# Kernel optimization log

Hardware: AMD Instinct MI355X
Metric: run time of the kernel (lower is better)

Reference implementation:

```python
import jax, jax.numpy as jnp
import numpy as np

KERNEL_SIZE = 4  # kernel_size=4, dim=1, degree-1 open B-splines (SplineConv defaults)


def spline_conv(x, edge_index, edge_attr, W, root, bias):
    """SplineConv with dim=1, kernel_size=4, degree=1, open splines, aggr='mean'.

    x: [N, F_in]; edge_index: [2, E] (row 0 = source, row 1 = target);
    edge_attr: [E, 1] pseudo-coords in [0,1]; W: [K, F_in, F_out];
    root: [F_in, F_out]; bias: [F_out].
    """
    N = x.shape[0]
    src, dst = edge_index[0], edge_index[1]
    u = edge_attr[:, 0]                          # [E]
    v = u * (KERNEL_SIZE - 1)                    # open spline: scale by K-1
    vf = jnp.floor(v)
    frac = v - vf                                # [E], degree-1 basis fraction
    k0 = jnp.clip(vf.astype(jnp.int32), 0, KERNEL_SIZE - 1)
    k1 = jnp.minimum(k0 + 1, KERNEL_SIZE - 1)
    # Project node features through all K kernel weights once: [N, K, F_out]
    xw = jnp.einsum('nf,kfo->nko', x, W)
    # Per-edge message: basis-weighted mix of the two active kernel projections
    m = (1.0 - frac)[:, None] * xw[src, k0] + frac[:, None] * xw[src, k1]  # [E, F_out]
    # Mean aggregation at target nodes
    agg = jax.ops.segment_sum(m, dst, num_segments=N)               # [N, F_out]
    deg = jax.ops.segment_sum(jnp.ones_like(u), dst, num_segments=N)
    agg = agg / jnp.maximum(deg, 1.0)[:, None]
    return agg + x @ root + bias


def setup_inputs() -> dict:
    key = jax.random.key(0)
    ks = jax.random.split(key, 9)
    N, E, F_IN, HID, C = 50000, 1600000, 48, 32, 10
    x = jax.random.normal(ks[0], (N, F_IN), dtype=jnp.float32)
    edge_index = jax.random.randint(ks[1], (2, E), 0, N, dtype=jnp.int64)
    edge_attr = jax.random.uniform(ks[2], (E, 1), dtype=jnp.float32)
    s = 0.1
    W1 = jax.random.normal(ks[3], (KERNEL_SIZE, F_IN, HID), dtype=jnp.float32) * s
    root1 = jax.random.normal(ks[4], (F_IN, HID), dtype=jnp.float32) * s
    bias1 = jax.random.normal(ks[5], (HID,), dtype=jnp.float32) * s
    W2 = jax.random.normal(ks[6], (KERNEL_SIZE, HID, C), dtype=jnp.float32) * s
    root2 = jax.random.normal(ks[7], (HID, C), dtype=jnp.float32) * s
    bias2 = jax.random.normal(ks[8], (C,), dtype=jnp.float32) * s
    return {"x": x, "edge_index": edge_index, "edge_attr": edge_attr,
            "W1": W1, "root1": root1, "bias1": bias1,
            "W2": W2, "root2": root2, "bias2": bias2}


def reference(x, edge_index, edge_attr, W1, root1, bias1, W2, root2, bias2):
    # dropout is identity in eval mode (training=self.training)
    h = spline_conv(x, edge_index, edge_attr, W1, root1, bias1)
    h = jax.nn.elu(h)
    h = spline_conv(h, edge_index, edge_attr, W2, root2, bias2)
    return jax.nn.log_softmax(h, axis=1)
```

## Files before the change

### kernel.cpp

```cpp
#include <hip/hip_runtime.h>
#include <math.h>


#define F_IN   48
#define HID    32
#define NCLS   10
#define KS     4
#define BKT_SH 8
#define TILE   4096

__device__ inline unsigned short f2bf(float f) {
    unsigned x = __float_as_uint(f);
    unsigned r = x + 0x7FFFu + ((x >> 16) & 1u);
    return (unsigned short)(r >> 16);
}
__device__ inline float bf2f(unsigned short u) {
    return __uint_as_float(((unsigned)u) << 16);
}


__global__ void bucket_hist_kernel(const int* __restrict__ ei, int* __restrict__ bcnt,
                                   int E, int NB) {
    __shared__ int lcnt[256];
    int t = threadIdx.x;
    lcnt[t] = 0;
    __syncthreads();
    int e0 = blockIdx.x * TILE;
    int n = min(TILE, E - e0);
    for (int r = 0; r < TILE / 256; ++r) {
        int i = r * 256 + t;
        if (i < n) atomicAdd(&lcnt[ei[E + e0 + i] >> BKT_SH], 1);
    }
    __syncthreads();
    if (t < NB && lcnt[t] > 0) atomicAdd(&bcnt[t], lcnt[t]);
}

__global__ void mini_scan_kernel(const int* __restrict__ bcnt, int* __restrict__ bbase,
                                 int* __restrict__ gcur, int NB) {
    __shared__ int a[256], c[256];
    int t = threadIdx.x;
    int v = (t < NB) ? bcnt[t] : 0;
    a[t] = v; c[t] = v;
    __syncthreads();
    for (int o = 1; o < 256; o <<= 1) {
        int w = (t >= o) ? a[t - o] : 0;
        __syncthreads();
        a[t] += w;
        __syncthreads();
    }
    int ex = a[t] - c[t];
    if (t < NB) { bbase[t] = ex; gcur[t] = ex; }
    if (t == 0) bbase[NB] = a[255];
}

__global__ void bucket_scatter_kernel(const int* __restrict__ ei, const float* __restrict__ ea,
                                      int* __restrict__ gcur, uint2* __restrict__ tpd,
                                      int E, int NB) {
    __shared__ unsigned spl[TILE];
    __shared__ unsigned short sdst[TILE];
    __shared__ unsigned short inv[TILE];
    __shared__ int lcnt[256], loff[256], lrank[256], gb[256];
    int t = threadIdx.x;
    lcnt[t] = 0; lrank[t] = 0;
    __syncthreads();
    int e0 = blockIdx.x * TILE;
    int n = min(TILE, E - e0);
    for (int r = 0; r < TILE / 256; ++r) {
        int i = r * 256 + t;
        if (i < n) {
            int e = e0 + i;
            int src = ei[e];
            int dst = ei[E + e];
            float u = ea[e];
            float v = u * (float)(KS - 1);
            float vf = floorf(v);
            int k0 = min(max((int)vf, 0), KS - 1);
            unsigned qf = (unsigned)((v - vf) * 16383.f + 0.5f);
            spl[i] = (unsigned)src | ((unsigned)k0 << 16) | (qf << 18);
            sdst[i] = (unsigned short)dst;
            atomicAdd(&lcnt[dst >> BKT_SH], 1);
        }
    }
    __syncthreads();
    loff[t] = lcnt[t];
    __syncthreads();
    for (int o = 1; o < 256; o <<= 1) {
        int w = (t >= o) ? loff[t - o] : 0;
        __syncthreads();
        loff[t] += w;
        __syncthreads();
    }
    int ex = loff[t] - lcnt[t];
    __syncthreads();
    loff[t] = ex;
    if (t < NB) gb[t] = atomicAdd(&gcur[t], lcnt[t]);
    __syncthreads();
    for (int r = 0; r < TILE / 256; ++r) {
        int i = r * 256 + t;
        if (i < n) {
            int b = sdst[i] >> BKT_SH;
            int p = loff[b] + atomicAdd(&lrank[b], 1);
            inv[p] = (unsigned short)i;
        }
    }
    __syncthreads();
    for (int r = 0; r < TILE / 256; ++r) {
        int j = r * 256 + t;
        if (j < n) {
            int i = inv[j];
            int d = sdst[i];
            int b = d >> BKT_SH;
            int pos = gb[b] + (j - loff[b]);
            tpd[pos] = make_uint2(spl[i], (unsigned)d);
        }
    }
}

__global__ void node_sort_kernel(const uint2* __restrict__ tpd, const int* __restrict__ bbase,
                                 unsigned* __restrict__ spk, int* __restrict__ offs,
                                 int N, int NB) {
    __shared__ int hc[256], hs[256], hr[256];
    int b = blockIdx.x;
    int t = threadIdx.x;
    int nb0 = b << BKT_SH;
    int nb = min(256, N - nb0);
    int base = bbase[b];
    int m = bbase[b + 1] - base;
    hc[t] = 0; hr[t] = 0;
    __syncthreads();
    for (int i = t; i < m; i += 256) atomicAdd(&hc[tpd[base + i].y - nb0], 1);
    __syncthreads();
    hs[t] = hc[t];
    __syncthreads();
    for (int o = 1; o < 256; o <<= 1) {
        int w = (t >= o) ? hs[t - o] : 0;
        __syncthreads();
        hs[t] += w;
        __syncthreads();
    }
    if (t < nb) offs[nb0 + t] = base + (hs[t] - hc[t]);
    if (b == NB - 1 && t == 0) offs[N] = base + m;
    for (int i = t; i < m; i += 256) {
        uint2 rec = tpd[base + i];
        int d = rec.y - nb0;
        int p = (hs[d] - hc[d]) + atomicAdd(&hr[d], 1);
        spk[base + p] = rec.x;
    }
}


__global__ __launch_bounds__(320) void xw1_kernel(
        const float* __restrict__ X, const float* __restrict__ W,
        const float* __restrict__ R, unsigned short* __restrict__ outk,
        float* __restrict__ outr, int n) {
    __shared__ float lw[48 * 160];
    int t = threadIdx.x;
    for (int i = t; i < 48 * 160; i += 320) {
        int f = i / 160;
        int col = i - f * 160;
        lw[i] = (col < 128) ? W[(size_t)(col >> 5) * (48 * 32) + f * 32 + (col & 31)]
                            : R[f * 32 + (col - 128)];
    }
    __syncthreads();
    int g = t % 40;
    int lp = t / 40;
    int n0 = (blockIdx.x * 8 + lp) * 2;
    if (n0 + 1 >= n) return;
    const float4* X0 = (const float4*)(X + (size_t)n0 * F_IN);
    const float4* X1 = (const float4*)(X + (size_t)(n0 + 1) * F_IN);
    float4 x0[12], x1[12];
#pragma unroll
    for (int i = 0; i < 12; ++i) { x0[i] = X0[i]; x1[i] = X1[i]; }
    const float4* lw4 = (const float4*)lw;
    float4 a0 = {0,0,0,0}, a1 = {0,0,0,0};
#pragma unroll
    for (int fb = 0; fb < 12; ++fb) {
        float4 v0 = x0[fb], v1 = x1[fb];
#pragma unroll
        for (int j = 0; j < 4; ++j) {
            float s0 = (j == 0) ? v0.x : (j == 1) ? v0.y : (j == 2) ? v0.z : v0.w;
            float s1 = (j == 0) ? v1.x : (j == 1) ? v1.y : (j == 2) ? v1.z : v1.w;
            float4 w = lw4[(fb * 4 + j) * 40 + g];
            a0.x = fmaf(s0, w.x, a0.x); a0.y = fmaf(s0, w.y, a0.y);
            a0.z = fmaf(s0, w.z, a0.z); a0.w = fmaf(s0, w.w, a0.w);
            a1.x = fmaf(s1, w.x, a1.x); a1.y = fmaf(s1, w.y, a1.y);
            a1.z = fmaf(s1, w.z, a1.z); a1.w = fmaf(s1, w.w, a1.w);
        }
    }
    if (g < 32) {
        uint2 u0, u1;
        u0.x = f2bf(a0.x) | ((unsigned)f2bf(a0.y) << 16);
        u0.y = f2bf(a0.z) | ((unsigned)f2bf(a0.w) << 16);
        u1.x = f2bf(a1.x) | ((unsigned)f2bf(a1.y) << 16);
        u1.y = f2bf(a1.z) | ((unsigned)f2bf(a1.w) << 16);
        *(uint2*)(outk + (size_t)n0 * (KS * HID) + g * 4) = u0;
        *(uint2*)(outk + (size_t)(n0 + 1) * (KS * HID) + g * 4) = u1;
    } else {
        int o = 4 * g - 128;
        *(float4*)(outr + (size_t)n0 * HID + o) = a0;
        *(float4*)(outr + (size_t)(n0 + 1) * HID + o) = a1;
    }
}

__global__ void xw2_kernel(const float* __restrict__ H, const float* __restrict__ W,
                           const float* __restrict__ R, unsigned short* __restrict__ outk,
                           float* __restrict__ outr, int n) {
    __shared__ float lw2[32 * 50];
    int t = threadIdx.x;
    for (int i = t; i < 32 * 50; i += 256) {
        int f = i / 50;
        int col = i - f * 50;
        lw2[i] = (col < 40) ? W[(size_t)(col / 10) * (32 * 10) + f * 10 + (col % 10)]
                            : R[f * 10 + (col - 40)];
    }
    __syncthreads();
    int total = (n / 2) * 25;
    int id = blockIdx.x * blockDim.x + t;
    if (id >= total) return;
    int p = id % 25;
    int pr = id / 25;
    int n0 = 2 * pr;
    const float4* H0 = (const float4*)(H + (size_t)n0 * HID);
    const float4* H1 = (const float4*)(H + (size_t)(n0 + 1) * HID);
    float4 h0[8], h1[8];
#pragma unroll
    for (int i = 0; i < 8; ++i) { h0[i] = H0[i]; h1[i] = H1[i]; }
    const float2* lwp = (const float2*)lw2;
    float ax0 = 0.f, ay0 = 0.f, ax1 = 0.f, ay1 = 0.f;
#pragma unroll
    for (int fb = 0; fb < 8; ++fb) {
        float4 v0 = h0[fb], v1 = h1[fb];
#pragma unroll
        for (int j = 0; j < 4; ++j) {
            float s0 = (j == 0) ? v0.x : (j == 1) ? v0.y : (j == 2) ? v0.z : v0.w;
            float s1 = (j == 0) ? v1.x : (j == 1) ? v1.y : (j == 2) ? v1.z : v1.w;
            float2 w = lwp[(fb * 4 + j) * 25 + p];
            ax0 = fmaf(s0, w.x, ax0); ay0 = fmaf(s0, w.y, ay0);
            ax1 = fmaf(s1, w.x, ax1); ay1 = fmaf(s1, w.y, ay1);
        }
    }
    int col = 2 * p;
    if (col < KS * NCLS) {
        *(unsigned*)(outk + (size_t)n0 * (KS * NCLS) + col) =
            f2bf(ax0) | ((unsigned)f2bf(ay0) << 16);
        *(unsigned*)(outk + (size_t)(n0 + 1) * (KS * NCLS) + col) =
            f2bf(ax1) | ((unsigned)f2bf(ay1) << 16);
    } else {
        int o = col - KS * NCLS;
        *(float2*)(outr + (size_t)n0 * NCLS + o) = make_float2(ax0, ay0);
        *(float2*)(outr + (size_t)(n0 + 1) * NCLS + o) = make_float2(ax1, ay1);
    }
}


__device__ inline float interp32(const unsigned short* __restrict__ xwk, unsigned p, int c) {
    int src = p & 0xFFFF;
    int k0 = (p >> 16) & 3;
    int k1 = min(k0 + 1, KS - 1);
    float fr = (float)(p >> 18) * (1.f / 16383.f);
    const unsigned short* row = xwk + (size_t)src * (KS * HID);
    float v0 = bf2f(row[k0 * HID + c]);
    float v1 = bf2f(row[k1 * HID + c]);
    return fmaf(fr, v1 - v0, v0);
}

__global__ void agg1_kernel(const unsigned short* __restrict__ xwk,
                            const float* __restrict__ xroot,
                            const int* __restrict__ offs, const unsigned* __restrict__ spk,
                            const float* __restrict__ bias, float* __restrict__ h, int n) {
    int lane = threadIdx.x & 63;
    int c = lane & 31;
    int half = lane >> 5;
    int node = blockIdx.x * 4 + (threadIdx.x >> 6);
    if (node >= n) return;
    int beg = offs[node];
    int end = offs[node + 1];
    float s0 = 0.f, s1 = 0.f;
    int e = beg + half;
    while (e + 2 < end) {
        unsigned p0 = spk[e];
        unsigned p1 = spk[e + 2];
        s0 += interp32(xwk, p0, c);
        s1 += interp32(xwk, p1, c);
        e += 4;
    }
    if (e < end) s0 += interp32(xwk, spk[e], c);
    float sum = s0 + s1;
    sum += __shfl_xor(sum, 32, 64);
    int deg = end - beg;
    float m = sum / (float)(deg > 0 ? deg : 1);
    float o = m + xroot[(size_t)node * HID + c] + bias[c];
    if (half == 0) h[(size_t)node * HID + c] = (o > 0.f) ? o : expm1f(o);
}

__device__ inline float interp10(const unsigned short* __restrict__ xwk, unsigned p, int cc) {
    int src = p & 0xFFFF;
    int k0 = (p >> 16) & 3;
    int k1 = min(k0 + 1, KS - 1);
    float fr = (float)(p >> 18) * (1.f / 16383.f);
    const unsigned short* row = xwk + (size_t)src * (KS * NCLS);
    float v0 = bf2f(row[k0 * NCLS + cc]);
    float v1 = bf2f(row[k1 * NCLS + cc]);
    return fmaf(fr, v1 - v0, v0);
}

__global__ void agg2_kernel(const unsigned short* __restrict__ xwk,
                            const float* __restrict__ xroot,
                            const int* __restrict__ offs, const unsigned* __restrict__ spk,
                            const float* __restrict__ bias, float* __restrict__ out, int n) {
    int g = threadIdx.x & 31;
    int c = g & 15;
    int par = g >> 4;
    int node = blockIdx.x * 8 + (threadIdx.x >> 5);
    if (node >= n) return;
    int cc = min(c, NCLS - 1);
    int beg = offs[node];
    int end = offs[node + 1];
    float s0 = 0.f, s1 = 0.f;
    int e = beg + par;
    while (e + 2 < end) {
        unsigned p0 = spk[e];
        unsigned p1 = spk[e + 2];
        s0 += interp10(xwk, p0, cc);
        s1 += interp10(xwk, p1, cc);
        e += 4;
    }
    if (e < end) s0 += interp10(xwk, spk[e], cc);
    float sum = s0 + s1;
    sum += __shfl_xor(sum, 16, 32);
    int deg = end - beg;
    float m = sum / (float)(deg > 0 ? deg : 1);
    float logit = m + xroot[(size_t)node * NCLS + cc] + bias[cc];
    bool active = (c < NCLS);
    float mx = active ? logit : -INFINITY;
#pragma unroll
    for (int msk = 1; msk < 16; msk <<= 1) mx = fmaxf(mx, __shfl_xor(mx, msk, 16));
    float ex = active ? expf(logit - mx) : 0.f;
    float s = ex;
#pragma unroll
    for (int msk = 1; msk < 16; msk <<= 1) s += __shfl_xor(s, msk, 16);
    if (active && par == 0) out[(size_t)node * NCLS + c] = (logit - mx) - logf(s);
}

extern "C" void kernel_launch(void* const* d_in, const int* in_sizes, int n_in,
                              void* d_out, int out_size, void* d_ws, size_t ws_size,
                              hipStream_t stream) {
    const float* x       = (const float*)d_in[0];
    const int*   ei      = (const int*)d_in[1];
    const float* ea      = (const float*)d_in[2];
    const float* W1      = (const float*)d_in[3];
    const float* root1   = (const float*)d_in[4];
    const float* bias1   = (const float*)d_in[5];
    const float* W2      = (const float*)d_in[6];
    const float* root2   = (const float*)d_in[7];
    const float* bias2   = (const float*)d_in[8];
    float* out = (float*)d_out;

    const int N = in_sizes[0] / F_IN;
    const int E = in_sizes[2];
    const int NB = (N + 255) >> BKT_SH;

    char* base = (char*)d_ws;
    size_t off = 0;
    auto alloc = [&](size_t bytes) {
        char* p = base + off;
        off = (off + bytes + 255) & ~(size_t)255;
        return (void*)p;
    };
    unsigned short* xwk1 = (unsigned short*)alloc((size_t)N * KS * HID * 2);
    float* xr1           = (float*)alloc((size_t)N * HID * 4);
    float* h             = (float*)alloc((size_t)N * HID * 4);
    int* offs            = (int*)alloc(((size_t)N + 1) * 4);
    int* bcnt            = (int*)alloc((size_t)NB * 4);
    int* bbase           = (int*)alloc(((size_t)NB + 1) * 4);
    int* gcur            = (int*)alloc((size_t)NB * 4);
    unsigned* spk        = (unsigned*)alloc((size_t)E * 4);
    uint2* tpd           = (uint2*)xwk1;
    unsigned short* xwk2 = xwk1;
    float* xr2           = xr1;
    if (ws_size < off) return;

    int ebk = (E + TILE - 1) / TILE;

    hipMemsetAsync(bcnt, 0, (size_t)NB * 4, stream);
    bucket_hist_kernel<<<ebk, 256, 0, stream>>>(ei, bcnt, E, NB);
    mini_scan_kernel<<<1, 256, 0, stream>>>(bcnt, bbase, gcur, NB);
    bucket_scatter_kernel<<<ebk, 256, 0, stream>>>(ei, ea, gcur, tpd, E, NB);
    node_sort_kernel<<<NB, 256, 0, stream>>>(tpd, bbase, spk, offs, N, NB);
    xw1_kernel<<<(N + 15) / 16, 320, 0, stream>>>(x, W1, root1, xwk1, xr1, N);
    agg1_kernel<<<(N + 3) / 4, 256, 0, stream>>>(xwk1, xr1, offs, spk, bias1, h, N);
    {
        int total = (N / 2) * 25;
        xw2_kernel<<<(total + 255) / 256, 256, 0, stream>>>(h, W2, root2, xwk2, xr2, N);
    }
    agg2_kernel<<<(N + 7) / 8, 256, 0, stream>>>(xwk2, xr2, offs, spk, bias2, out, N);
}
```

Before: 266.7 us.

## Drop per-node sort; aggregate bucketed edges with shared-memory atomics per block

Removes the node_sort pass that built a CSR layout. Both aggregation kernels now run one 1024-thread block per 256-node bucket, read the bucketed edge records directly, and accumulate messages into shared-memory tiles with atomic adds. Degrees are counted in the first pass and reused in the second. This saves a sort pass and the CSR indirection, but adds heavy LDS atomic contention and gives only 196 blocks, so the GPU may be underfilled. The edge buffer now needs its own workspace allocation instead of aliasing xwk1.

```diff
diff --git a/kernel.cpp b/kernel.cpp
--- a/kernel.cpp
+++ b/kernel.cpp
@@ -116,38 +116,6 @@
     }
 }
 
-__global__ void node_sort_kernel(const uint2* __restrict__ tpd, const int* __restrict__ bbase,
-                                 unsigned* __restrict__ spk, int* __restrict__ offs,
-                                 int N, int NB) {
-    __shared__ int hc[256], hs[256], hr[256];
-    int b = blockIdx.x;
-    int t = threadIdx.x;
-    int nb0 = b << BKT_SH;
-    int nb = min(256, N - nb0);
-    int base = bbase[b];
-    int m = bbase[b + 1] - base;
-    hc[t] = 0; hr[t] = 0;
-    __syncthreads();
-    for (int i = t; i < m; i += 256) atomicAdd(&hc[tpd[base + i].y - nb0], 1);
-    __syncthreads();
-    hs[t] = hc[t];
-    __syncthreads();
-    for (int o = 1; o < 256; o <<= 1) {
-        int w = (t >= o) ? hs[t - o] : 0;
-        __syncthreads();
-        hs[t] += w;
-        __syncthreads();
-    }
-    if (t < nb) offs[nb0 + t] = base + (hs[t] - hc[t]);
-    if (b == NB - 1 && t == 0) offs[N] = base + m;
-    for (int i = t; i < m; i += 256) {
-        uint2 rec = tpd[base + i];
-        int d = rec.y - nb0;
-        int p = (hs[d] - hc[d]) + atomicAdd(&hr[d], 1);
-        spk[base + p] = rec.x;
-    }
-}
-
 
 __global__ __launch_bounds__(320) void xw1_kernel(
         const float* __restrict__ X, const float* __restrict__ W,
@@ -253,93 +221,218 @@
 }
 
 
-__device__ inline float interp32(const unsigned short* __restrict__ xwk, unsigned p, int c) {
-    int src = p & 0xFFFF;
-    int k0 = (p >> 16) & 3;
-    int k1 = min(k0 + 1, KS - 1);
-    float fr = (float)(p >> 18) * (1.f / 16383.f);
-    const unsigned short* row = xwk + (size_t)src * (KS * HID);
-    float v0 = bf2f(row[k0 * HID + c]);
-    float v1 = bf2f(row[k1 * HID + c]);
-    return fmaf(fr, v1 - v0, v0);
-}
-
-__global__ void agg1_kernel(const unsigned short* __restrict__ xwk,
-                            const float* __restrict__ xroot,
-                            const int* __restrict__ offs, const unsigned* __restrict__ spk,
-                            const float* __restrict__ bias, float* __restrict__ h, int n) {
-    int lane = threadIdx.x & 63;
-    int c = lane & 31;
-    int half = lane >> 5;
-    int node = blockIdx.x * 4 + (threadIdx.x >> 6);
-    if (node >= n) return;
-    int beg = offs[node];
-    int end = offs[node + 1];
-    float s0 = 0.f, s1 = 0.f;
-    int e = beg + half;
-    while (e + 2 < end) {
-        unsigned p0 = spk[e];
-        unsigned p1 = spk[e + 2];
-        s0 += interp32(xwk, p0, c);
-        s1 += interp32(xwk, p1, c);
-        e += 4;
-    }
-    if (e < end) s0 += interp32(xwk, spk[e], c);
-    float sum = s0 + s1;
-    sum += __shfl_xor(sum, 32, 64);
-    int deg = end - beg;
-    float m = sum / (float)(deg > 0 ? deg : 1);
-    float o = m + xroot[(size_t)node * HID + c] + bias[c];
-    if (half == 0) h[(size_t)node * HID + c] = (o > 0.f) ? o : expm1f(o);
-}
-
-__device__ inline float interp10(const unsigned short* __restrict__ xwk, unsigned p, int cc) {
-    int src = p & 0xFFFF;
-    int k0 = (p >> 16) & 3;
-    int k1 = min(k0 + 1, KS - 1);
-    float fr = (float)(p >> 18) * (1.f / 16383.f);
-    const unsigned short* row = xwk + (size_t)src * (KS * NCLS);
-    float v0 = bf2f(row[k0 * NCLS + cc]);
-    float v1 = bf2f(row[k1 * NCLS + cc]);
-    return fmaf(fr, v1 - v0, v0);
-}
-
-__global__ void agg2_kernel(const unsigned short* __restrict__ xwk,
-                            const float* __restrict__ xroot,
-                            const int* __restrict__ offs, const unsigned* __restrict__ spk,
-                            const float* __restrict__ bias, float* __restrict__ out, int n) {
-    int g = threadIdx.x & 31;
-    int c = g & 15;
-    int par = g >> 4;
-    int node = blockIdx.x * 8 + (threadIdx.x >> 5);
-    if (node >= n) return;
-    int cc = min(c, NCLS - 1);
-    int beg = offs[node];
-    int end = offs[node + 1];
-    float s0 = 0.f, s1 = 0.f;
-    int e = beg + par;
-    while (e + 2 < end) {
-        unsigned p0 = spk[e];
-        unsigned p1 = spk[e + 2];
-        s0 += interp10(xwk, p0, cc);
-        s1 += interp10(xwk, p1, cc);
-        e += 4;
-    }
-    if (e < end) s0 += interp10(xwk, spk[e], cc);
-    float sum = s0 + s1;
-    sum += __shfl_xor(sum, 16, 32);
-    int deg = end - beg;
-    float m = sum / (float)(deg > 0 ? deg : 1);
-    float logit = m + xroot[(size_t)node * NCLS + cc] + bias[cc];
-    bool active = (c < NCLS);
-    float mx = active ? logit : -INFINITY;
-#pragma unroll
-    for (int msk = 1; msk < 16; msk <<= 1) mx = fmaxf(mx, __shfl_xor(mx, msk, 16));
-    float ex = active ? expf(logit - mx) : 0.f;
-    float s = ex;
-#pragma unroll
-    for (int msk = 1; msk < 16; msk <<= 1) s += __shfl_xor(s, msk, 16);
-    if (active && par == 0) out[(size_t)node * NCLS + c] = (logit - mx) - logf(s);
+__global__ __launch_bounds__(1024) void agg1b_kernel(
+        const uint2* __restrict__ tpd, const int* __restrict__ bbase,
+        const unsigned short* __restrict__ xwk, const float* __restrict__ xroot,
+        const float* __restrict__ bias, float* __restrict__ h,
+        int* __restrict__ deg_g, int N) {
+    __shared__ float acc[256 * 33];
+    __shared__ int degc[256];
+    int t = threadIdx.x;
+    for (int i = t; i < 256 * 33; i += 1024) acc[i] = 0.f;
+    if (t < 256) degc[t] = 0;
+    __syncthreads();
+    int b = blockIdx.x;
+    int nb0 = b << BKT_SH;
+    int base = bbase[b];
+    int m = bbase[b + 1] - base;
+    int s = t >> 3;
+    int cg = t & 7;
+    int idx = s;
+    while (idx + 128 * 7 < m) {
+        uint2 rec[8];
+#pragma unroll
+        for (int k = 0; k < 8; ++k) rec[k] = tpd[base + idx + 128 * k];
+        const unsigned short* row[8];
+        int dk[8], dl[8];
+        float fr[8];
+#pragma unroll
+        for (int k = 0; k < 8; ++k) {
+            unsigned p = rec[k].x;
+            dl[k] = rec[k].y & 255;
+            int src = p & 0xFFFF;
+            int k0 = (p >> 16) & 3;
+            int k1 = min(k0 + 1, KS - 1);
+            fr[k] = (float)(p >> 18) * (1.f / 16383.f);
+            row[k] = xwk + (size_t)src * (KS * HID) + k0 * HID + cg * 4;
+            dk[k] = (k1 - k0) * HID;
+        }
+        uint2 v0[8], v1[8];
+#pragma unroll
+        for (int k = 0; k < 8; ++k) {
+            v0[k] = *(const uint2*)row[k];
+            v1[k] = *(const uint2*)(row[k] + dk[k]);
+        }
+#pragma unroll
+        for (int k = 0; k < 8; ++k) {
+            float w0 = 1.f - fr[k];
+            float* ap = &acc[dl[k] * 33 + cg * 4];
+            atomicAdd(ap + 0, fmaf(w0, __uint_as_float(v0[k].x << 16),
+                                   fr[k] * __uint_as_float(v1[k].x << 16)));
+            atomicAdd(ap + 1, fmaf(w0, __uint_as_float(v0[k].x & 0xFFFF0000u),
+                                   fr[k] * __uint_as_float(v1[k].x & 0xFFFF0000u)));
+            atomicAdd(ap + 2, fmaf(w0, __uint_as_float(v0[k].y << 16),
+                                   fr[k] * __uint_as_float(v1[k].y << 16)));
+            atomicAdd(ap + 3, fmaf(w0, __uint_as_float(v0[k].y & 0xFFFF0000u),
+                                   fr[k] * __uint_as_float(v1[k].y & 0xFFFF0000u)));
+            if (cg == 0) atomicAdd(&degc[dl[k]], 1);
+        }
+        idx += 1024;
+    }
+    while (idx < m) {
+        uint2 rec = tpd[base + idx];
+        unsigned p = rec.x;
+        int dl = rec.y & 255;
+        int src = p & 0xFFFF;
+        int k0 = (p >> 16) & 3;
+        int k1 = min(k0 + 1, KS - 1);
+        float fr = (float)(p >> 18) * (1.f / 16383.f);
+        const unsigned short* row = xwk + (size_t)src * (KS * HID) + k0 * HID + cg * 4;
+        uint2 v0 = *(const uint2*)row;
+        uint2 v1 = *(const uint2*)(row + (k1 - k0) * HID);
+        float w0 = 1.f - fr;
+        float* ap = &acc[dl * 33 + cg * 4];
+        atomicAdd(ap + 0, fmaf(w0, __uint_as_float(v0.x << 16),
+                               fr * __uint_as_float(v1.x << 16)));
+        atomicAdd(ap + 1, fmaf(w0, __uint_as_float(v0.x & 0xFFFF0000u),
+                               fr * __uint_as_float(v1.x & 0xFFFF0000u)));
+        atomicAdd(ap + 2, fmaf(w0, __uint_as_float(v0.y << 16),
+                               fr * __uint_as_float(v1.y << 16)));
+        atomicAdd(ap + 3, fmaf(w0, __uint_as_float(v0.y & 0xFFFF0000u),
+                               fr * __uint_as_float(v1.y & 0xFFFF0000u)));
+        if (cg == 0) atomicAdd(&degc[dl], 1);
+        idx += 128;
+    }
+    __syncthreads();
+    int nl = t >> 2;
+    int q = t & 3;
+    int node = nb0 + nl;
+    if (node < N) {
+        int dg = degc[nl];
+        float inv = 1.f / (float)(dg > 0 ? dg : 1);
+        const float* ap = &acc[nl * 33 + q * 8];
+        float4 r0 = *(const float4*)(xroot + (size_t)node * HID + q * 8);
+        float4 r1 = *(const float4*)(xroot + (size_t)node * HID + q * 8 + 4);
+        float4 b0 = *(const float4*)(bias + q * 8);
+        float4 b1 = *(const float4*)(bias + q * 8 + 4);
+        float4 o0, o1;
+        o0.x = fmaf(ap[0], inv, r0.x + b0.x);
+        o0.y = fmaf(ap[1], inv, r0.y + b0.y);
+        o0.z = fmaf(ap[2], inv, r0.z + b0.z);
+        o0.w = fmaf(ap[3], inv, r0.w + b0.w);
+        o1.x = fmaf(ap[4], inv, r1.x + b1.x);
+        o1.y = fmaf(ap[5], inv, r1.y + b1.y);
+        o1.z = fmaf(ap[6], inv, r1.z + b1.z);
+        o1.w = fmaf(ap[7], inv, r1.w + b1.w);
+        o0.x = (o0.x > 0.f) ? o0.x : expm1f(o0.x);
+        o0.y = (o0.y > 0.f) ? o0.y : expm1f(o0.y);
+        o0.z = (o0.z > 0.f) ? o0.z : expm1f(o0.z);
+        o0.w = (o0.w > 0.f) ? o0.w : expm1f(o0.w);
+        o1.x = (o1.x > 0.f) ? o1.x : expm1f(o1.x);
+        o1.y = (o1.y > 0.f) ? o1.y : expm1f(o1.y);
+        o1.z = (o1.z > 0.f) ? o1.z : expm1f(o1.z);
+        o1.w = (o1.w > 0.f) ? o1.w : expm1f(o1.w);
+        *(float4*)(h + (size_t)node * HID + q * 8) = o0;
+        *(float4*)(h + (size_t)node * HID + q * 8 + 4) = o1;
+        if (q == 0) deg_g[node] = dg;
+    }
+}
+
+__global__ __launch_bounds__(1024) void agg2b_kernel(
+        const uint2* __restrict__ tpd, const int* __restrict__ bbase,
+        const unsigned short* __restrict__ xwk, const float* __restrict__ xroot,
+        const float* __restrict__ bias, const int* __restrict__ deg_g,
+        float* __restrict__ out, int N) {
+    __shared__ float acc[256 * 11];
+    int t = threadIdx.x;
+    for (int i = t; i < 256 * 11; i += 1024) acc[i] = 0.f;
+    __syncthreads();
+    int b = blockIdx.x;
+    int nb0 = b << BKT_SH;
+    int base = bbase[b];
+    int m = bbase[b + 1] - base;
+    int s = t >> 3;
+    int u = t & 7;
+    if (u < 5) {
+        int idx = s;
+        while (idx + 128 * 3 < m) {
+            uint2 rec[4];
+#pragma unroll
+            for (int k = 0; k < 4; ++k) rec[k] = tpd[base + idx + 128 * k];
+            const unsigned *q0[4], *q1[4];
+            int dl[4];
+            float fr[4];
+#pragma unroll
+            for (int k = 0; k < 4; ++k) {
+                unsigned p = rec[k].x;
+                dl[k] = rec[k].y & 255;
+                int src = p & 0xFFFF;
+                int k0 = (p >> 16) & 3;
+                int k1 = min(k0 + 1, KS - 1);
+                fr[k] = (float)(p >> 18) * (1.f / 16383.f);
+                const unsigned short* row = xwk + (size_t)src * 40;
+                q0[k] = (const unsigned*)(row + k0 * 10) + u;
+                q1[k] = (const unsigned*)(row + k1 * 10) + u;
+            }
+            unsigned t0[4], t1[4];
+#pragma unroll
+            for (int k = 0; k < 4; ++k) { t0[k] = *q0[k]; t1[k] = *q1[k]; }
+#pragma unroll
+            for (int k = 0; k < 4; ++k) {
+                float w0 = 1.f - fr[k];
+                float lo = fmaf(w0, __uint_as_float(t0[k] << 16),
+                                fr[k] * __uint_as_float(t1[k] << 16));
+                float hi = fmaf(w0, __uint_as_float(t0[k] & 0xFFFF0000u),
+                                fr[k] * __uint_as_float(t1[k] & 0xFFFF0000u));
+                atomicAdd(&acc[dl[k] * 11 + 2 * u], lo);
+                atomicAdd(&acc[dl[k] * 11 + 2 * u + 1], hi);
+            }
+            idx += 512;
+        }
+        while (idx < m) {
+            uint2 rec = tpd[base + idx];
+            unsigned p = rec.x;
+            int dl = rec.y & 255;
+            int src = p & 0xFFFF;
+            int k0 = (p >> 16) & 3;
+            int k1 = min(k0 + 1, KS - 1);
+            float fr = (float)(p >> 18) * (1.f / 16383.f);
+            const unsigned short* row = xwk + (size_t)src * 40;
+            unsigned t0 = *((const unsigned*)(row + k0 * 10) + u);
+            unsigned t1 = *((const unsigned*)(row + k1 * 10) + u);
+            float w0 = 1.f - fr;
+            float lo = fmaf(w0, __uint_as_float(t0 << 16),
+                            fr * __uint_as_float(t1 << 16));
+            float hi = fmaf(w0, __uint_as_float(t0 & 0xFFFF0000u),
+                            fr * __uint_as_float(t1 & 0xFFFF0000u));
+            atomicAdd(&acc[dl * 11 + 2 * u], lo);
+            atomicAdd(&acc[dl * 11 + 2 * u + 1], hi);
+            idx += 128;
+        }
+    }
+    __syncthreads();
+    if (t < 256) {
+        int node = nb0 + t;
+        if (node < N) {
+            int dg = deg_g[node];
+            float inv = 1.f / (float)(dg > 0 ? dg : 1);
+            float l[NCLS];
+            float mx = -INFINITY;
+#pragma unroll
+            for (int c = 0; c < NCLS; ++c) {
+                l[c] = fmaf(acc[t * 11 + c], inv,
+                            xroot[(size_t)node * NCLS + c] + bias[c]);
+                mx = fmaxf(mx, l[c]);
+            }
+            float sden = 0.f;
+#pragma unroll
+            for (int c = 0; c < NCLS; ++c) sden += expf(l[c] - mx);
+            float ls = logf(sden);
+#pragma unroll
+            for (int c = 0; c < NCLS; ++c)
+                out[(size_t)node * NCLS + c] = l[c] - mx - ls;
+        }
+    }
 }
 
 extern "C" void kernel_launch(void* const* d_in, const int* in_sizes, int n_in,
@@ -370,12 +463,11 @@
     unsigned short* xwk1 = (unsigned short*)alloc((size_t)N * KS * HID * 2);
     float* xr1           = (float*)alloc((size_t)N * HID * 4);
     float* h             = (float*)alloc((size_t)N * HID * 4);
-    int* offs            = (int*)alloc(((size_t)N + 1) * 4);
+    int* deg_g           = (int*)alloc((size_t)N * 4);
     int* bcnt            = (int*)alloc((size_t)NB * 4);
     int* bbase           = (int*)alloc(((size_t)NB + 1) * 4);
     int* gcur            = (int*)alloc((size_t)NB * 4);
-    unsigned* spk        = (unsigned*)alloc((size_t)E * 4);
-    uint2* tpd           = (uint2*)xwk1;
+    uint2* tpd           = (uint2*)alloc((size_t)E * 8);
     unsigned short* xwk2 = xwk1;
     float* xr2           = xr1;
     if (ws_size < off) return;
@@ -386,12 +478,11 @@
     bucket_hist_kernel<<<ebk, 256, 0, stream>>>(ei, bcnt, E, NB);
     mini_scan_kernel<<<1, 256, 0, stream>>>(bcnt, bbase, gcur, NB);
     bucket_scatter_kernel<<<ebk, 256, 0, stream>>>(ei, ea, gcur, tpd, E, NB);
-    node_sort_kernel<<<NB, 256, 0, stream>>>(tpd, bbase, spk, offs, N, NB);
     xw1_kernel<<<(N + 15) / 16, 320, 0, stream>>>(x, W1, root1, xwk1, xr1, N);
-    agg1_kernel<<<(N + 3) / 4, 256, 0, stream>>>(xwk1, xr1, offs, spk, bias1, h, N);
+    agg1b_kernel<<<NB, 1024, 0, stream>>>(tpd, bbase, xwk1, xr1, bias1, h, deg_g, N);
     {
         int total = (N / 2) * 25;
         xw2_kernel<<<(total + 255) / 256, 256, 0, stream>>>(h, W2, root2, xwk2, xr2, N);
     }
-    agg2_kernel<<<(N + 7) / 8, 256, 0, stream>>>(xwk2, xr2, offs, spk, bias2, out, N);
-}
+    agg2b_kernel<<<NB, 1024, 0, stream>>>(tpd, bbase, xwk2, xr2, bias2, deg_g, out, N);
+}
```

Result: slower. 615.5 us (+130.8%).
